# Performance work log

Hardware: AMD Instinct MI355X
Metric: run time of the kernel (lower is better)

Reference implementation:

```python
import jax, jax.numpy as jnp
import numpy as np
from jax import lax

B, T, I, H, L = 256, 512, 156, 128, 32


def setup_inputs() -> dict:
    key = jax.random.key(0)
    ks = jax.random.split(key, 16)
    kb = 1.0 / np.sqrt(H)  # torch default LSTM/Linear init bound

    def u(k, shape, bound):
        return jax.random.uniform(k, shape, minval=-bound, maxval=bound, dtype=jnp.float32)

    return {
        "motion": jax.random.normal(ks[0], (B, T, I), dtype=jnp.float32),
        "eps": jax.random.normal(ks[1], (B, L), dtype=jnp.float32),
        # encoder LSTM (gate order i,f,g,o; b = b_ih + b_hh folded together)
        "enc_Wih": u(ks[2], (4 * H, I), kb),
        "enc_Whh": u(ks[3], (4 * H, H), kb),
        "enc_b": u(ks[4], (4 * H,), kb),
        "mu_W": u(ks[5], (L, H), kb),
        "mu_b": u(ks[6], (L,), kb),
        "var_W": u(ks[7], (L, H), kb),
        "var_b": u(ks[8], (L,), kb),
        # decoder
        "dec_fc_W": u(ks[9], (H, L), 1.0 / np.sqrt(L)),
        "dec_fc_b": u(ks[10], (H,), 1.0 / np.sqrt(L)),
        "dec_Wih": u(ks[11], (4 * H, H), kb),
        "dec_Whh": u(ks[12], (4 * H, H), kb),
        "dec_b": u(ks[13], (4 * H,), kb),
        "out_W": u(ks[14], (I, H), kb),
        "out_b": u(ks[15], (I,), kb),
    }


def _cell(gates, c):
    # PyTorch LSTM gate layout: [i, f, g, o] along the 4H axis
    i, f, g, o = jnp.split(gates, 4, axis=-1)
    c_new = jax.nn.sigmoid(f) * c + jax.nn.sigmoid(i) * jnp.tanh(g)
    h_new = jax.nn.sigmoid(o) * jnp.tanh(c_new)
    return h_new, c_new


def reference(motion, eps, enc_Wih, enc_Whh, enc_b, mu_W, mu_b, var_W, var_b,
              dec_fc_W, dec_fc_b, dec_Wih, dec_Whh, dec_b, out_W, out_b):
    b, t, _ = motion.shape

    # ---- encoder LSTM: single scan over time, keep only final hidden ----
    def enc_step(carry, x_t):
        h, c = carry
        gates = x_t @ enc_Wih.T + h @ enc_Whh.T + enc_b
        h, c = _cell(gates, c)
        return (h, c), None

    h0 = jnp.zeros((b, H), motion.dtype)
    c0 = jnp.zeros((b, H), motion.dtype)
    (h_fin, _), _ = lax.scan(enc_step, (h0, c0), jnp.swapaxes(motion, 0, 1))

    mu = h_fin @ mu_W.T + mu_b          # [B, L]
    logvar = h_fin @ var_W.T + var_b    # [B, L] ('var' in the torch code)

    # ---- reparameterize ----
    z = mu + eps * jnp.exp(0.5 * logvar)

    # ---- decoder: input at each step is the previous hidden state ----
    dh0 = z @ dec_fc_W.T + dec_fc_b     # [B, H]
    dc0 = jnp.zeros((b, H), motion.dtype)

    def dec_step(carry, _):
        h, c = carry
        gates = h @ dec_Wih.T + h @ dec_Whh.T + dec_b
        h, c = _cell(gates, c)
        return (h, c), h

    _, hs = lax.scan(dec_step, (dh0, dc0), None, length=t)  # [T, B, H]
    recon = jnp.einsum('tbh,oh->bto', hs, out_W) + out_b    # [B, T, I]

    # ---- losses ----
    rec_loss = jnp.mean((recon - motion) ** 2)
    kl_loss = -0.5 * jnp.sum(1.0 + logvar - mu ** 2 - jnp.exp(logvar))
    total = rec_loss + kl_loss
    return recon, mu, logvar, total
```

## Files before the change

kernel.cpp:

```cpp
#include <hip/hip_runtime.h>
#include <hip/hip_fp16.h>

#define B_ 256
#define T_ 512
#define I_ 156
#define H_ 128
#define L_ 32
#define G_ 512

typedef _Float16 half_t;
typedef _Float16 h2_t __attribute__((ext_vector_type(2)));

union U8 { uint4 u; h2_t h2[4]; };

__device__ __forceinline__ float fdot2(h2_t a, h2_t b, float c) {
#if __has_builtin(__builtin_amdgcn_fdot2)
  return __builtin_amdgcn_fdot2(a, b, c, false);
#else
  return c + (float)a[0] * (float)b[0] + (float)a[1] * (float)b[1];
#endif
}

__device__ __forceinline__ h2_t pk2(float a, float b) {
  h2_t r; r[0] = (half_t)a; r[1] = (half_t)b; return r;
}

__device__ __forceinline__ float sigf(float x) { return 1.0f / (1.0f + __expf(-x)); }
__device__ __forceinline__ float tanhf_(float x) {
  x = fminf(fmaxf(x, -20.f), 20.f);
  float e = __expf(2.f * x);
  return (e - 1.f) / (e + 1.f);
}

__global__ __launch_bounds__(1024, 4) void enc_kernel(
    const float* __restrict__ motion, const float* __restrict__ eps,
    const float* __restrict__ Wih, const float* __restrict__ Whh,
    const float* __restrict__ bv,
    const float* __restrict__ muW, const float* __restrict__ mub,
    const float* __restrict__ varW, const float* __restrict__ varb,
    const float* __restrict__ fcW, const float* __restrict__ fcb,
    float* __restrict__ dout, float* __restrict__ dh0,
    float* __restrict__ accums)
{
  const int tid  = threadIdx.x;
  const int part = tid >> 9;
  const int j    = tid & 511;
  const int b    = blockIdx.x;

  __shared__ h2_t xs[2][80];
  __shared__ h2_t hs[64];
  __shared__ float gl2[2][G_];
  __shared__ float hf[H_];
  __shared__ float mulv[64];
  __shared__ float zs[L_];

  h2_t wih[40];
  h2_t whh[32];
  {
    const int cbase = part * 80;
    const float* wr = Wih + (size_t)j * I_;
#pragma unroll
    for (int k = 0; k < 40; ++k) {
      int c0 = cbase + 2 * k;
      float a = (c0     < I_) ? wr[c0]     : 0.f;
      float c = (c0 + 1 < I_) ? wr[c0 + 1] : 0.f;
      wih[k] = pk2(a, c);
    }
    const float2* r2 = (const float2*)(Whh + (size_t)j * H_ + part * 64);
#pragma unroll
    for (int k = 0; k < 32; ++k) { float2 w = r2[k]; whh[k] = pk2(w.x, w.y); }
  }

  float cb0 = 0.f, cb1 = 0.f, cb2 = 0.f, cb3 = 0.f;
  if (tid < H_) {
    cb0 = bv[tid]; cb1 = bv[tid + H_]; cb2 = bv[tid + 2*H_]; cb3 = bv[tid + 3*H_];
  }

  float creg = 0.f, hreg = 0.f;
  if (tid < 64) hs[tid] = pk2(0.f, 0.f);
  if (tid < 4)  xs[tid >> 1][78 + (tid & 1)] = pk2(0.f, 0.f);

  const float2* mrow = (const float2*)(motion + (size_t)b * T_ * I_);
  const bool loader = (part == 1) && (j < 78);
  if (loader) { float2 m = mrow[j]; xs[0][j] = pk2(m.x, m.y); }
  __syncthreads();

  int cur = 0;
  float2 xreg;
  for (int t = 0; t < T_; ++t) {
    if (loader && t + 1 < T_) xreg = mrow[(t + 1) * 78 + j];

    float a0 = 0.f, a1 = 0.f, a2 = 0.f, a3 = 0.f;
    const U8* xv = (const U8*)&xs[cur][part * 40];
#pragma unroll
    for (int c = 0; c < 10; ++c) {
      U8 v = xv[c];
      a0 = fdot2(wih[4*c+0], v.h2[0], a0);
      a1 = fdot2(wih[4*c+1], v.h2[1], a1);
      a2 = fdot2(wih[4*c+2], v.h2[2], a2);
      a3 = fdot2(wih[4*c+3], v.h2[3], a3);
    }
    const U8* hv = (const U8*)&hs[part * 32];
#pragma unroll
    for (int c = 0; c < 8; ++c) {
      U8 v = hv[c];
      a0 = fdot2(whh[4*c+0], v.h2[0], a0);
      a1 = fdot2(whh[4*c+1], v.h2[1], a1);
      a2 = fdot2(whh[4*c+2], v.h2[2], a2);
      a3 = fdot2(whh[4*c+3], v.h2[3], a3);
    }
    gl2[part][j] = (a0 + a1) + (a2 + a3);
    if (loader && t + 1 < T_) xs[cur ^ 1][j] = pk2(xreg.x, xreg.y);
    __syncthreads();

    if (tid < H_) {
      float ig = gl2[0][tid]         + gl2[1][tid]         + cb0;
      float fg = gl2[0][tid +   H_]  + gl2[1][tid +   H_]  + cb1;
      float gg = gl2[0][tid + 2*H_]  + gl2[1][tid + 2*H_]  + cb2;
      float og = gl2[0][tid + 3*H_]  + gl2[1][tid + 3*H_]  + cb3;
      creg = sigf(fg) * creg + sigf(ig) * tanhf_(gg);
      hreg = sigf(og) * tanhf_(creg);
      ((half_t*)hs)[tid] = (half_t)hreg;
    }
    __syncthreads();
    cur ^= 1;
  }

  if (tid < H_) hf[tid] = hreg;
  __syncthreads();

  if (tid < 64) {
    const float* wr = (tid < L_) ? (muW + tid * H_) : (varW + (tid - L_) * H_);
    float a = (tid < L_) ? mub[tid] : varb[tid - L_];
#pragma unroll 8
    for (int k = 0; k < H_; ++k) a += wr[k] * hf[k];
    mulv[tid] = a;
    if (tid < L_) dout[(size_t)B_*T_*I_ + b * L_ + tid] = a;
    else          dout[(size_t)B_*T_*I_ + B_*L_ + b * L_ + (tid - L_)] = a;
  }
  __syncthreads();

  if (tid < L_) {
    float mu = mulv[tid], lv = mulv[tid + L_];
    float z = mu + eps[b * L_ + tid] * __expf(0.5f * lv);
    zs[tid] = z;
    float kt = 1.f + lv - mu * mu - __expf(lv);
#pragma unroll
    for (int off = 16; off > 0; off >>= 1) kt += __shfl_down(kt, off, 64);
    if (tid == 0) atomicAdd(&accums[1], kt);
  }
  __syncthreads();

  if (tid < H_) {
    const float* wr = fcW + tid * L_;
    float a = fcb[tid];
#pragma unroll
    for (int l = 0; l < L_; ++l) a += wr[l] * zs[l];
    dh0[b * H_ + tid] = a;
  }
}

__global__ __launch_bounds__(1024, 4) void dec_kernel(
    const float* __restrict__ motion,
    const float* __restrict__ Wih, const float* __restrict__ Whh,
    const float* __restrict__ bv,
    const float* __restrict__ oW, const float* __restrict__ ob,
    const float* __restrict__ dh0,
    float* __restrict__ dout, float* __restrict__ accums)
{
  const int tid  = threadIdx.x;
  const int part = tid >> 9;
  const int j    = tid & 511;
  const int b    = blockIdx.x;

  __shared__ h2_t hs[64];
  __shared__ float gl[G_];
  __shared__ float red[16];

  h2_t wv[64];
  float bj = 0.f;
  if (part == 0) {
    const float2* r1 = (const float2*)(Wih + (size_t)j * H_);
    const float2* r2 = (const float2*)(Whh + (size_t)j * H_);
#pragma unroll
    for (int k = 0; k < 64; ++k) {
      float2 a = r1[k], c = r2[k];
      wv[k] = pk2(a.x + c.x, a.y + c.y);
    }
    bj = bv[j];
  } else if (j < I_) {
    const float2* r = (const float2*)(oW + (size_t)j * H_);
#pragma unroll
    for (int k = 0; k < 64; ++k) { float2 w = r[k]; wv[k] = pk2(w.x, w.y); }
    bj = ob[j];
  }

  float creg = 0.f, hreg = 0.f;
  if (tid < H_) {
    hreg = dh0[b * H_ + tid];
    ((half_t*)hs)[tid] = (half_t)hreg;
  }
  __syncthreads();

  const float* mr = motion + (size_t)b * T_ * I_;
  float* rr = dout + (size_t)b * T_ * I_;
  float rl = 0.f;

  for (int t = 0; t < T_; ++t) {
    if (part == 0) {
      float a0 = 0.f, a1 = 0.f, a2 = 0.f, a3 = 0.f;
      const U8* hv = (const U8*)hs;
#pragma unroll
      for (int c = 0; c < 16; ++c) {
        U8 v = hv[c];
        a0 = fdot2(wv[4*c+0], v.h2[0], a0);
        a1 = fdot2(wv[4*c+1], v.h2[1], a1);
        a2 = fdot2(wv[4*c+2], v.h2[2], a2);
        a3 = fdot2(wv[4*c+3], v.h2[3], a3);
      }
      gl[j] = bj + (a0 + a1) + (a2 + a3);
    } else if (j < I_ && t > 0) {
      float a0 = 0.f, a1 = 0.f, a2 = 0.f, a3 = 0.f;
      const U8* hv = (const U8*)hs;
#pragma unroll
      for (int c = 0; c < 16; ++c) {
        U8 v = hv[c];
        a0 = fdot2(wv[4*c+0], v.h2[0], a0);
        a1 = fdot2(wv[4*c+1], v.h2[1], a1);
        a2 = fdot2(wv[4*c+2], v.h2[2], a2);
        a3 = fdot2(wv[4*c+3], v.h2[3], a3);
      }
      float r = bj + (a0 + a1) + (a2 + a3);
      rr[(t - 1) * I_ + j] = r;
      float d = r - mr[(t - 1) * I_ + j];
      rl += d * d;
    }
    __syncthreads();

    if (tid < H_) {
      float ig = gl[tid], fg = gl[tid + H_], gg = gl[tid + 2*H_], og = gl[tid + 3*H_];
      creg = sigf(fg) * creg + sigf(ig) * tanhf_(gg);
      hreg = sigf(og) * tanhf_(creg);
      ((half_t*)hs)[tid] = (half_t)hreg;
    }
    __syncthreads();
  }

  if (part == 1 && j < I_) {
    float a0 = 0.f, a1 = 0.f, a2 = 0.f, a3 = 0.f;
    const U8* hv = (const U8*)hs;
#pragma unroll
    for (int c = 0; c < 16; ++c) {
      U8 v = hv[c];
      a0 = fdot2(wv[4*c+0], v.h2[0], a0);
      a1 = fdot2(wv[4*c+1], v.h2[1], a1);
      a2 = fdot2(wv[4*c+2], v.h2[2], a2);
      a3 = fdot2(wv[4*c+3], v.h2[3], a3);
    }
    float r = bj + (a0 + a1) + (a2 + a3);
    rr[511 * I_ + j] = r;
    float d = r - mr[511 * I_ + j];
    rl += d * d;
  }

  float v = rl;
#pragma unroll
  for (int off = 32; off > 0; off >>= 1) v += __shfl_down(v, off, 64);
  if ((tid & 63) == 0) red[tid >> 6] = v;
  __syncthreads();
  if (tid == 0) {
    float s = 0.f;
#pragma unroll
    for (int w = 0; w < 16; ++w) s += red[w];
    atomicAdd(&accums[0], s);
  }
}

__global__ void init_kernel(float* accums) {
  if (threadIdx.x < 2) accums[threadIdx.x] = 0.f;
}

__global__ void fin_kernel(const float* __restrict__ accums, float* __restrict__ dout) {
  if (threadIdx.x == 0) {
    float rec = accums[0] / (float)((size_t)B_ * T_ * I_);
    float kl = -0.5f * accums[1];
    dout[(size_t)B_*T_*I_ + 2 * B_ * L_] = rec + kl;
  }
}

extern "C" void kernel_launch(void* const* d_in, const int* in_sizes, int n_in,
                              void* d_out, int out_size, void* d_ws, size_t ws_size,
                              hipStream_t stream) {
  const float* motion = (const float*)d_in[0];
  const float* eps    = (const float*)d_in[1];
  const float* eWih   = (const float*)d_in[2];
  const float* eWhh   = (const float*)d_in[3];
  const float* eb     = (const float*)d_in[4];
  const float* muW    = (const float*)d_in[5];
  const float* mub    = (const float*)d_in[6];
  const float* varW   = (const float*)d_in[7];
  const float* varb   = (const float*)d_in[8];
  const float* fcW    = (const float*)d_in[9];
  const float* fcb    = (const float*)d_in[10];
  const float* dWih   = (const float*)d_in[11];
  const float* dWhh   = (const float*)d_in[12];
  const float* db     = (const float*)d_in[13];
  const float* oW     = (const float*)d_in[14];
  const float* obv    = (const float*)d_in[15];
  float* out = (float*)d_out;
  float* accums = (float*)d_ws;
  float* dh0    = (float*)d_ws + 16;

  hipLaunchKernelGGL(init_kernel, dim3(1), dim3(64), 0, stream, accums);
  hipLaunchKernelGGL(enc_kernel, dim3(B_), dim3(1024), 0, stream,
                     motion, eps, eWih, eWhh, eb, muW, mub, varW, varb, fcW, fcb,
                     out, dh0, accums);
  hipLaunchKernelGGL(dec_kernel, dim3(B_), dim3(1024), 0, stream,
                     motion, dWih, dWhh, db, oW, obv, dh0, out, accums);
  hipLaunchKernelGGL(fin_kernel, dim3(1), dim3(64), 0, stream, accums, out);
}
```

Measured before the change: 1.162 ms.

## Restructure LSTM VAE into MFMA-based input projection, batched recurrences, and output projection

```diff
diff --git a/kernel.cpp b/kernel.cpp
--- a/kernel.cpp
+++ b/kernel.cpp
@@ -10,6 +10,8 @@
 
 typedef _Float16 half_t;
 typedef _Float16 h2_t __attribute__((ext_vector_type(2)));
+typedef _Float16 f16x8 __attribute__((ext_vector_type(8)));
+typedef float f32x4 __attribute__((ext_vector_type(4)));
 
 union U8 { uint4 u; h2_t h2[4]; };
 
@@ -32,7 +34,408 @@
   return (e - 1.f) / (e + 1.f);
 }
 
-__global__ __launch_bounds__(1024, 4) void enc_kernel(
+__device__ __forceinline__ f32x4 mfma16(f16x8 a, f16x8 b, f32x4 c) {
+  return __builtin_amdgcn_mfma_f32_16x16x32_f16(a, b, c, 0, 0, 0);
+}
+
+__device__ __forceinline__ f16x8 load_bfrag(const float* __restrict__ W, int row,
+                                            int ld, int kbase, int kmax) {
+  f16x8 r;
+#pragma unroll
+  for (int j = 0; j < 8; ++j) {
+    int k = kbase + j;
+    r[j] = (half_t)((k < kmax) ? W[(size_t)row * ld + k] : 0.f);
+  }
+  return r;
+}
+
+__global__ __launch_bounds__(512, 2) void xproj_mfma(
+    const float* __restrict__ motion, const float* __restrict__ Wih,
+    const float* __restrict__ bv, half_t* __restrict__ XP)
+{
+  const int tid = threadIdx.x, lane = tid & 63, wv = tid >> 6;
+  const int l15 = lane & 15, lg = lane >> 4;
+  const int b16 = blockIdx.x >> 4;
+  const int tc  = blockIdx.x & 15;
+
+  __shared__ half_t xA[128 * 160];
+
+  f16x8 fB[4][5];
+  float bn[4];
+#pragma unroll
+  for (int i = 0; i < 4; ++i) {
+    int n = (wv * 4 + i) * 16 + l15;
+    bn[i] = bv[n];
+#pragma unroll
+    for (int kk = 0; kk < 5; ++kk)
+      fB[i][kk] = load_bfrag(Wih, n, I_, kk * 32 + lg * 8, I_);
+  }
+  uint2* xout = (uint2*)XP;
+
+  for (int sc = 0; sc < 4; ++sc) {
+    const int t0 = tc * 32 + sc * 8;
+    {
+      int r = tid >> 2, q = tid & 3;
+      int tt = r >> 4, bb = r & 15;
+      const float* src = motion + ((size_t)(b16 * 16 + bb) * T_ + (t0 + tt)) * I_;
+#pragma unroll
+      for (int i2 = 0; i2 < 10; ++i2) {
+        int c4 = q * 10 + i2;
+        h2_t v0 = pk2(0.f, 0.f), v1 = pk2(0.f, 0.f);
+        if (c4 < 39) {
+          float4 m4 = *(const float4*)(src + c4 * 4);
+          v0 = pk2(m4.x, m4.y); v1 = pk2(m4.z, m4.w);
+        }
+        int idx = (r * 160 + c4 * 4) ^ ((bb & 7) << 3);
+        *(h2_t*)&xA[idx]     = v0;
+        *(h2_t*)&xA[idx + 2] = v1;
+      }
+    }
+    __syncthreads();
+    for (int tt = 0; tt < 8; ++tt) {
+      f16x8 fA[5];
+#pragma unroll
+      for (int kk = 0; kk < 5; ++kk) {
+        int row = tt * 16 + l15;
+        int idx = (row * 160 + kk * 32 + lg * 8) ^ ((l15 & 7) << 3);
+        fA[kk] = *(const f16x8*)&xA[idx];
+      }
+      const int t = t0 + tt;
+#pragma unroll
+      for (int i = 0; i < 4; ++i) {
+        f32x4 acc = {bn[i], bn[i], bn[i], bn[i]};
+#pragma unroll
+        for (int kk = 0; kk < 5; ++kk) acc = mfma16(fA[kk], fB[i][kk], acc);
+        uint2 o; half_t* oh = (half_t*)&o;
+#pragma unroll
+        for (int r = 0; r < 4; ++r) oh[r] = (half_t)acc[r];
+        xout[((size_t)(b16 * 32 + wv * 4 + i) * T_ + t) * 64 + lane] = o;
+      }
+    }
+    __syncthreads();
+  }
+}
+
+__global__ __launch_bounds__(512, 2) void enc_mfma(
+    const half_t* __restrict__ XP, const float* __restrict__ Whh,
+    const float* __restrict__ eps,
+    const float* __restrict__ muW, const float* __restrict__ mub,
+    const float* __restrict__ varW, const float* __restrict__ varb,
+    const float* __restrict__ fcW, const float* __restrict__ fcb,
+    float* __restrict__ dout, float* __restrict__ dh0g,
+    float* __restrict__ accums)
+{
+  const int tid = threadIdx.x, lane = tid & 63, wv = tid >> 6;
+  const int l15 = lane & 15, lg = lane >> 4;
+  const int b16 = blockIdx.x;
+
+  __shared__ half_t hA[2048];
+  __shared__ float  gl[8192];
+  __shared__ float  hf[2048];
+  __shared__ float  mulv[1024];
+  __shared__ float  zs[512];
+  __shared__ float  red[8];
+
+  f16x8 fB[4][4];
+#pragma unroll
+  for (int i = 0; i < 4; ++i) {
+    int n = (wv * 4 + i) * 16 + l15;
+#pragma unroll
+    for (int kk = 0; kk < 4; ++kk)
+      fB[i][kk] = load_bfrag(Whh, n, H_, kk * 32 + lg * 8, H_);
+  }
+
+  ((uint2*)hA)[tid] = make_uint2(0u, 0u);
+  float cc[4] = {0.f, 0.f, 0.f, 0.f};
+  float hr[4] = {0.f, 0.f, 0.f, 0.f};
+
+  const uint2* xptr = (const uint2*)XP;
+  int xbase[4];
+#pragma unroll
+  for (int i = 0; i < 4; ++i)
+    xbase[i] = ((b16 * 32 + wv * 4 + i) * T_) * 64 + lane;
+  uint2 xpv[2][4];
+#pragma unroll
+  for (int i = 0; i < 4; ++i) {
+    xpv[0][i] = xptr[xbase[i]];
+    xpv[1][i] = xptr[xbase[i] + 64];
+  }
+
+  const int m_c = tid >> 7;
+  const int h_c = tid & 127;
+
+  __syncthreads();
+
+  for (int t = 0; t < T_; ++t) {
+    const int cur = t & 1;
+    f16x8 fA[4];
+#pragma unroll
+    for (int kk = 0; kk < 4; ++kk) {
+      int idx = (l15 * 128 + kk * 32 + lg * 8) ^ ((l15 & 7) << 3);
+      fA[kk] = *(const f16x8*)&hA[idx];
+    }
+#pragma unroll
+    for (int i = 0; i < 4; ++i) {
+      const half_t* xh = (const half_t*)&xpv[cur][i];
+      f32x4 acc;
+#pragma unroll
+      for (int r = 0; r < 4; ++r) acc[r] = (float)xh[r];
+#pragma unroll
+      for (int kk = 0; kk < 4; ++kk) acc = mfma16(fA[kk], fB[i][kk], acc);
+      int n = (wv * 4 + i) * 16 + l15;
+      int gidx = (n * 16 + lg * 4) ^ ((n & 7) << 2);
+      *(f32x4*)&gl[gidx] = acc;
+    }
+    if (t + 2 < T_) {
+#pragma unroll
+      for (int i = 0; i < 4; ++i)
+        xpv[cur][i] = xptr[xbase[i] + (t + 2) * 64];
+    }
+    asm volatile("s_waitcnt lgkmcnt(0)" ::: "memory");
+    __builtin_amdgcn_s_barrier();
+    __builtin_amdgcn_sched_barrier(0);
+#pragma unroll
+    for (int p = 0; p < 4; ++p) {
+      int m = m_c + p * 4;
+      int sw = (h_c & 7) << 2;
+      float ig = gl[(h_c * 16 + m) ^ sw];
+      float fg = gl[((h_c + 128) * 16 + m) ^ sw];
+      float gg = gl[((h_c + 256) * 16 + m) ^ sw];
+      float og = gl[((h_c + 384) * 16 + m) ^ sw];
+      float c2 = sigf(fg) * cc[p] + sigf(ig) * tanhf_(gg);
+      cc[p] = c2;
+      float hv = sigf(og) * tanhf_(c2);
+      hr[p] = hv;
+      hA[(m * 128 + h_c) ^ ((m & 7) << 3)] = (half_t)hv;
+    }
+    asm volatile("s_waitcnt lgkmcnt(0)" ::: "memory");
+    __builtin_amdgcn_s_barrier();
+    __builtin_amdgcn_sched_barrier(0);
+  }
+
+#pragma unroll
+  for (int p = 0; p < 4; ++p) hf[(m_c + p * 4) * 128 + h_c] = hr[p];
+  __syncthreads();
+  {
+    int b = tid >> 5, oo = tid & 31;
+    const float* h0 = &hf[b * 128];
+    float am = mub[oo], av = varb[oo];
+    const float* wm = &muW[oo * H_];
+    const float* wvv = &varW[oo * H_];
+    for (int k = 0; k < H_; ++k) { float hv = h0[k]; am += wm[k] * hv; av += wvv[k] * hv; }
+    mulv[b * 64 + oo] = am;
+    mulv[b * 64 + 32 + oo] = av;
+    int bg = b16 * 16 + b;
+    dout[(size_t)B_ * T_ * I_ + bg * L_ + oo] = am;
+    dout[(size_t)B_ * T_ * I_ + B_ * L_ + bg * L_ + oo] = av;
+  }
+  __syncthreads();
+  float kt;
+  {
+    int b = tid >> 5, l = tid & 31;
+    float mu = mulv[b * 64 + l], lv = mulv[b * 64 + 32 + l];
+    int bg = b16 * 16 + b;
+    float z = mu + eps[bg * L_ + l] * __expf(0.5f * lv);
+    zs[b * 32 + l] = z;
+    kt = 1.f + lv - mu * mu - __expf(lv);
+  }
+#pragma unroll
+  for (int off = 32; off > 0; off >>= 1) kt += __shfl_down(kt, off, 64);
+  if (lane == 0) red[wv] = kt;
+  __syncthreads();
+  if (tid == 0) {
+    float s = 0.f;
+#pragma unroll
+    for (int w = 0; w < 8; ++w) s += red[w];
+    atomicAdd(&accums[1], s);
+  }
+  {
+    int b = tid >> 5, hb = (tid & 31) * 4;
+    int bg = b16 * 16 + b;
+#pragma unroll
+    for (int q = 0; q < 4; ++q) {
+      int hh = hb + q;
+      float a = fcb[hh];
+      const float* wr = &fcW[hh * L_];
+#pragma unroll
+      for (int l = 0; l < L_; ++l) a += wr[l] * zs[b * 32 + l];
+      dh0g[(size_t)bg * H_ + hh] = a;
+    }
+  }
+}
+
+__global__ __launch_bounds__(512, 2) void dec_mfma(
+    const float* __restrict__ Wih, const float* __restrict__ Whh,
+    const float* __restrict__ bv, const float* __restrict__ dh0g,
+    half_t* __restrict__ hist)
+{
+  const int tid = threadIdx.x, lane = tid & 63, wv = tid >> 6;
+  const int l15 = lane & 15, lg = lane >> 4;
+  const int b16 = blockIdx.x;
+
+  __shared__ half_t hA[2048];
+  __shared__ float  gl[8192];
+
+  f16x8 fB[4][4];
+  float bn[4];
+#pragma unroll
+  for (int i = 0; i < 4; ++i) {
+    int n = (wv * 4 + i) * 16 + l15;
+    bn[i] = bv[n];
+#pragma unroll
+    for (int kk = 0; kk < 4; ++kk) {
+      f16x8 r;
+#pragma unroll
+      for (int j = 0; j < 8; ++j) {
+        int k = kk * 32 + lg * 8 + j;
+        r[j] = (half_t)(Wih[(size_t)n * H_ + k] + Whh[(size_t)n * H_ + k]);
+      }
+      fB[i][kk] = r;
+    }
+  }
+
+  const int m_c = tid >> 7;
+  const int h_c = tid & 127;
+
+  float cc[4] = {0.f, 0.f, 0.f, 0.f};
+  half_t* hp[4];
+#pragma unroll
+  for (int p = 0; p < 4; ++p) {
+    int m = m_c + p * 4;
+    float h0 = dh0g[(size_t)(b16 * 16 + m) * H_ + h_c];
+    hA[(m * 128 + h_c) ^ ((m & 7) << 3)] = (half_t)h0;
+    hp[p] = hist + ((size_t)(b16 * 16 + m) * T_) * H_ + h_c;
+  }
+  __syncthreads();
+
+  for (int t = 0; t < T_; ++t) {
+    f16x8 fA[4];
+#pragma unroll
+    for (int kk = 0; kk < 4; ++kk) {
+      int idx = (l15 * 128 + kk * 32 + lg * 8) ^ ((l15 & 7) << 3);
+      fA[kk] = *(const f16x8*)&hA[idx];
+    }
+#pragma unroll
+    for (int i = 0; i < 4; ++i) {
+      f32x4 acc = {bn[i], bn[i], bn[i], bn[i]};
+#pragma unroll
+      for (int kk = 0; kk < 4; ++kk) acc = mfma16(fA[kk], fB[i][kk], acc);
+      int n = (wv * 4 + i) * 16 + l15;
+      int gidx = (n * 16 + lg * 4) ^ ((n & 7) << 2);
+      *(f32x4*)&gl[gidx] = acc;
+    }
+    asm volatile("s_waitcnt lgkmcnt(0)" ::: "memory");
+    __builtin_amdgcn_s_barrier();
+    __builtin_amdgcn_sched_barrier(0);
+#pragma unroll
+    for (int p = 0; p < 4; ++p) {
+      int m = m_c + p * 4;
+      int sw = (h_c & 7) << 2;
+      float ig = gl[(h_c * 16 + m) ^ sw];
+      float fg = gl[((h_c + 128) * 16 + m) ^ sw];
+      float gg = gl[((h_c + 256) * 16 + m) ^ sw];
+      float og = gl[((h_c + 384) * 16 + m) ^ sw];
+      float c2 = sigf(fg) * cc[p] + sigf(ig) * tanhf_(gg);
+      cc[p] = c2;
+      float hv = sigf(og) * tanhf_(c2);
+      half_t hvh = (half_t)hv;
+      hA[(m * 128 + h_c) ^ ((m & 7) << 3)] = hvh;
+      hp[p][t * H_] = hvh;
+    }
+    asm volatile("s_waitcnt lgkmcnt(0)" ::: "memory");
+    __builtin_amdgcn_s_barrier();
+    __builtin_amdgcn_sched_barrier(0);
+  }
+}
+
+__global__ __launch_bounds__(512, 2) void proj_mfma(
+    const half_t* __restrict__ hist, const float* __restrict__ oW,
+    const float* __restrict__ ob, const float* __restrict__ motion,
+    float* __restrict__ recon, float* __restrict__ accums)
+{
+  const int tid = threadIdx.x, lane = tid & 63, wv = tid >> 6;
+  const int l15 = lane & 15, lg = lane >> 4;
+  const int R0 = blockIdx.x * 128;
+
+  __shared__ half_t xA[128 * 128];
+  __shared__ float red[8];
+
+  {
+    const uint4* src = (const uint4*)(hist + (size_t)R0 * H_);
+#pragma unroll
+    for (int q = 0; q < 4; ++q) {
+      int u = tid + q * 512;
+      int row = u >> 4, ccu = u & 15;
+      uint4 v = src[u];
+      int idx = (row * 128 + ccu * 8) ^ ((row & 7) << 3);
+      *(uint4*)&xA[idx] = v;
+    }
+  }
+  const int nt = (wv < 2) ? 2 : 1;
+  f16x8 fB[2][4];
+  float bn[2];
+  int   nn[2];
+#pragma unroll
+  for (int s = 0; s < 2; ++s) {
+    int tile = (s == 0) ? wv : wv + 8;
+    int n = tile * 16 + l15;
+    nn[s] = n;
+    bool valid = (s < nt) && (n < I_);
+    bn[s] = valid ? ob[n] : 0.f;
+#pragma unroll
+    for (int kk = 0; kk < 4; ++kk) {
+      f16x8 r;
+      if (valid) r = load_bfrag(oW, n, H_, kk * 32 + lg * 8, H_);
+      else {
+#pragma unroll
+        for (int j = 0; j < 8; ++j) r[j] = (half_t)0.f;
+      }
+      fB[s][kk] = r;
+    }
+  }
+  __syncthreads();
+
+  float rl = 0.f;
+  for (int mt = 0; mt < 8; ++mt) {
+    f16x8 fA[4];
+#pragma unroll
+    for (int kk = 0; kk < 4; ++kk) {
+      int idx = ((mt * 16 + l15) * 128 + kk * 32 + lg * 8) ^ ((l15 & 7) << 3);
+      fA[kk] = *(const f16x8*)&xA[idx];
+    }
+#pragma unroll
+    for (int s = 0; s < 2; ++s) {
+      if (s >= nt) break;
+      f32x4 acc = {bn[s], bn[s], bn[s], bn[s]};
+#pragma unroll
+      for (int kk = 0; kk < 4; ++kk) acc = mfma16(fA[kk], fB[s][kk], acc);
+      int n = nn[s];
+      if (n < I_) {
+#pragma unroll
+        for (int r = 0; r < 4; ++r) {
+          size_t grow = (size_t)R0 + mt * 16 + lg * 4 + r;
+          size_t a = grow * I_ + n;
+          float v = acc[r];
+          recon[a] = v;
+          float d = v - motion[a];
+          rl += d * d;
+        }
+      }
+    }
+  }
+#pragma unroll
+  for (int off = 32; off > 0; off >>= 1) rl += __shfl_down(rl, off, 64);
+  if (lane == 0) red[wv] = rl;
+  __syncthreads();
+  if (tid == 0) {
+    float s = 0.f;
+#pragma unroll
+    for (int w = 0; w < 8; ++w) s += red[w];
+    atomicAdd(&accums[0], s);
+  }
+}
+
+__global__ __launch_bounds__(1024) void enc_fb_kernel(
     const float* __restrict__ motion, const float* __restrict__ eps,
     const float* __restrict__ Wih, const float* __restrict__ Whh,
     const float* __restrict__ bv,
@@ -50,9 +453,9 @@
   __shared__ h2_t xs[2][80];
   __shared__ h2_t hs[64];
   __shared__ float gl2[2][G_];
-  __shared__ float hf[H_];
+  __shared__ float hfv[H_];
   __shared__ float mulv[64];
-  __shared__ float zs[L_];
+  __shared__ float zsv[L_];
 
   h2_t wih[40];
   h2_t whh[32];
@@ -70,26 +473,21 @@
 #pragma unroll
     for (int k = 0; k < 32; ++k) { float2 w = r2[k]; whh[k] = pk2(w.x, w.y); }
   }
-
   float cb0 = 0.f, cb1 = 0.f, cb2 = 0.f, cb3 = 0.f;
   if (tid < H_) {
     cb0 = bv[tid]; cb1 = bv[tid + H_]; cb2 = bv[tid + 2*H_]; cb3 = bv[tid + 3*H_];
   }
-
   float creg = 0.f, hreg = 0.f;
   if (tid < 64) hs[tid] = pk2(0.f, 0.f);
   if (tid < 4)  xs[tid >> 1][78 + (tid & 1)] = pk2(0.f, 0.f);
-
   const float2* mrow = (const float2*)(motion + (size_t)b * T_ * I_);
   const bool loader = (part == 1) && (j < 78);
   if (loader) { float2 m = mrow[j]; xs[0][j] = pk2(m.x, m.y); }
   __syncthreads();
-
   int cur = 0;
   float2 xreg;
   for (int t = 0; t < T_; ++t) {
     if (loader && t + 1 < T_) xreg = mrow[(t + 1) * 78 + j];
-
     float a0 = 0.f, a1 = 0.f, a2 = 0.f, a3 = 0.f;
     const U8* xv = (const U8*)&xs[cur][part * 40];
 #pragma unroll
@@ -112,12 +510,11 @@
     gl2[part][j] = (a0 + a1) + (a2 + a3);
     if (loader && t + 1 < T_) xs[cur ^ 1][j] = pk2(xreg.x, xreg.y);
     __syncthreads();
-
     if (tid < H_) {
-      float ig = gl2[0][tid]         + gl2[1][tid]         + cb0;
-      float fg = gl2[0][tid +   H_]  + gl2[1][tid +   H_]  + cb1;
-      float gg = gl2[0][tid + 2*H_]  + gl2[1][tid + 2*H_]  + cb2;
-      float og = gl2[0][tid + 3*H_]  + gl2[1][tid + 3*H_]  + cb3;
+      float ig = gl2[0][tid]        + gl2[1][tid]        + cb0;
+      float fg = gl2[0][tid +   H_] + gl2[1][tid +   H_] + cb1;
+      float gg = gl2[0][tid + 2*H_] + gl2[1][tid + 2*H_] + cb2;
+      float og = gl2[0][tid + 3*H_] + gl2[1][tid + 3*H_] + cb3;
       creg = sigf(fg) * creg + sigf(ig) * tanhf_(gg);
       hreg = sigf(og) * tanhf_(creg);
       ((half_t*)hs)[tid] = (half_t)hreg;
@@ -125,42 +522,38 @@
     __syncthreads();
     cur ^= 1;
   }
-
-  if (tid < H_) hf[tid] = hreg;
-  __syncthreads();
-
+  if (tid < H_) hfv[tid] = hreg;
+  __syncthreads();
   if (tid < 64) {
     const float* wr = (tid < L_) ? (muW + tid * H_) : (varW + (tid - L_) * H_);
     float a = (tid < L_) ? mub[tid] : varb[tid - L_];
 #pragma unroll 8
-    for (int k = 0; k < H_; ++k) a += wr[k] * hf[k];
+    for (int k = 0; k < H_; ++k) a += wr[k] * hfv[k];
     mulv[tid] = a;
     if (tid < L_) dout[(size_t)B_*T_*I_ + b * L_ + tid] = a;
     else          dout[(size_t)B_*T_*I_ + B_*L_ + b * L_ + (tid - L_)] = a;
   }
   __syncthreads();
-
   if (tid < L_) {
     float mu = mulv[tid], lv = mulv[tid + L_];
     float z = mu + eps[b * L_ + tid] * __expf(0.5f * lv);
-    zs[tid] = z;
+    zsv[tid] = z;
     float kt = 1.f + lv - mu * mu - __expf(lv);
 #pragma unroll
     for (int off = 16; off > 0; off >>= 1) kt += __shfl_down(kt, off, 64);
     if (tid == 0) atomicAdd(&accums[1], kt);
   }
   __syncthreads();
-
   if (tid < H_) {
     const float* wr = fcW + tid * L_;
     float a = fcb[tid];
 #pragma unroll
-    for (int l = 0; l < L_; ++l) a += wr[l] * zs[l];
+    for (int l = 0; l < L_; ++l) a += wr[l] * zsv[l];
     dh0[b * H_ + tid] = a;
   }
 }
 
-__global__ __launch_bounds__(1024, 4) void dec_kernel(
+__global__ __launch_bounds__(1024) void dec_fb_kernel(
     const float* __restrict__ motion,
     const float* __restrict__ Wih, const float* __restrict__ Whh,
     const float* __restrict__ bv,
@@ -194,18 +587,15 @@
     for (int k = 0; k < 64; ++k) { float2 w = r[k]; wv[k] = pk2(w.x, w.y); }
     bj = ob[j];
   }
-
   float creg = 0.f, hreg = 0.f;
   if (tid < H_) {
     hreg = dh0[b * H_ + tid];
     ((half_t*)hs)[tid] = (half_t)hreg;
   }
   __syncthreads();
-
   const float* mr = motion + (size_t)b * T_ * I_;
   float* rr = dout + (size_t)b * T_ * I_;
   float rl = 0.f;
-
   for (int t = 0; t < T_; ++t) {
     if (part == 0) {
       float a0 = 0.f, a1 = 0.f, a2 = 0.f, a3 = 0.f;
@@ -236,7 +626,6 @@
       rl += d * d;
     }
     __syncthreads();
-
     if (tid < H_) {
       float ig = gl[tid], fg = gl[tid + H_], gg = gl[tid + 2*H_], og = gl[tid + 3*H_];
       creg = sigf(fg) * creg + sigf(ig) * tanhf_(gg);
@@ -245,7 +634,6 @@
     }
     __syncthreads();
   }
-
   if (part == 1 && j < I_) {
     float a0 = 0.f, a1 = 0.f, a2 = 0.f, a3 = 0.f;
     const U8* hv = (const U8*)hs;
@@ -262,7 +650,6 @@
     float d = r - mr[511 * I_ + j];
     rl += d * d;
   }
-
   float v = rl;
 #pragma unroll
   for (int off = 32; off > 0; off >>= 1) v += __shfl_down(v, off, 64);
@@ -308,14 +695,32 @@
   const float* oW     = (const float*)d_in[14];
   const float* obv    = (const float*)d_in[15];
   float* out = (float*)d_out;
+
   float* accums = (float*)d_ws;
-  float* dh0    = (float*)d_ws + 16;
+  float* dh0    = (float*)((char*)d_ws + 256);
+  const size_t sh_off = 256 + 131072;
+  const size_t need = sh_off + (size_t)64 * 512 * 512 * 8;
+  const bool big = ws_size >= need;
+  half_t* XP   = (half_t*)((char*)d_ws + sh_off);
+  half_t* hist = XP;
 
   hipLaunchKernelGGL(init_kernel, dim3(1), dim3(64), 0, stream, accums);
-  hipLaunchKernelGGL(enc_kernel, dim3(B_), dim3(1024), 0, stream,
-                     motion, eps, eWih, eWhh, eb, muW, mub, varW, varb, fcW, fcb,
-                     out, dh0, accums);
-  hipLaunchKernelGGL(dec_kernel, dim3(B_), dim3(1024), 0, stream,
-                     motion, dWih, dWhh, db, oW, obv, dh0, out, accums);
+  if (big) {
+    hipLaunchKernelGGL(xproj_mfma, dim3(256), dim3(512), 0, stream,
+                       motion, eWih, eb, XP);
+    hipLaunchKernelGGL(enc_mfma, dim3(16), dim3(512), 0, stream,
+                       XP, eWhh, eps, muW, mub, varW, varb, fcW, fcb,
+                       out, dh0, accums);
+    hipLaunchKernelGGL(dec_mfma, dim3(16), dim3(512), 0, stream,
+                       dWih, dWhh, db, dh0, hist);
+    hipLaunchKernelGGL(proj_mfma, dim3(1024), dim3(512), 0, stream,
+                       hist, oW, obv, motion, out, accums);
+  } else {
+    hipLaunchKernelGGL(enc_fb_kernel, dim3(B_), dim3(1024), 0, stream,
+                       motion, eps, eWih, eWhh, eb, muW, mub, varW, varb, fcW, fcb,
+                       out, dh0, accums);
+    hipLaunchKernelGGL(dec_fb_kernel, dim3(B_), dim3(1024), 0, stream,
+                       motion, dWih, dWhh, db, oW, obv, dh0, out, accums);
+  }
   hipLaunchKernelGGL(fin_kernel, dim3(1), dim3(64), 0, stream, accums, out);
 }
```

After: 2.573 ms. 122% more time.
